# Optimization experiments

Measured on AMD Instinct MI355X. Metric: run time of the kernel, lower is better.

Reference implementation:

```python
import jax, jax.numpy as jnp
import numpy as np

B, L, E, H, NL = 2, 1024, 1024, 16, 3
D = E // H
SCALE = D ** -0.5
EPS = 1e-5


def rmsnorm(x, g):
    return x * jax.lax.rsqrt(jnp.mean(x * x, axis=-1, keepdims=True) + EPS) * g


def rope(x, cos, sin):
    # x: (B, m*L, H, D); cos/sin: (L, D). Tile cos/sin to the growing KV length
    # (the source broadcasts rel_pos over the concatenated cache).
    m = x.shape[1] // cos.shape[0]
    c = jnp.tile(cos, (m, 1))[None, :, None, :]
    s = jnp.tile(sin, (m, 1))[None, :, None, :]
    x1, x2 = jnp.split(x, 2, axis=-1)
    rot = jnp.concatenate([-x2, x1], axis=-1)  # rotate_half convention
    return x * c + rot * s


def setup_inputs() -> dict:
    key = jax.random.key(0)
    ks = jax.random.split(key, 8)
    x = jax.random.normal(ks[0], (B, L, E), jnp.float32)
    inv_freq = 1.0 / (10000.0 ** (jnp.arange(0, D, 2, dtype=jnp.float32) / D))
    t = jnp.arange(L, dtype=jnp.float32)[:, None] * inv_freq[None, :]  # (L, D/2)
    cos = jnp.concatenate([jnp.cos(t), jnp.cos(t)], axis=-1)
    sin = jnp.concatenate([jnp.sin(t), jnp.sin(t)], axis=-1)
    attn_mask = jnp.where(jnp.tril(jnp.ones((L, L), bool)), 0.0, -jnp.inf).astype(jnp.float32)
    w_scale = E ** -0.5  # ~kaiming_uniform fan_in magnitude
    Wq = jax.random.normal(ks[1], (NL, E, E), jnp.float32) * w_scale
    Wk = jax.random.normal(ks[2], (NL, E, E), jnp.float32) * w_scale
    Wv = jax.random.normal(ks[3], (NL, E, E), jnp.float32) * w_scale
    Wo = jax.random.normal(ks[4], (E, E), jnp.float32) * w_scale
    lambdas = jax.random.normal(ks[5], (NL,), jnp.float32)
    g_ln = jnp.ones((NL, E), jnp.float32)
    g_final = jnp.ones((E,), jnp.float32)
    alpha = jnp.ones((1,), jnp.float32)
    return dict(x=x, cos=cos, sin=sin, attn_mask=attn_mask, Wq=Wq, Wk=Wk, Wv=Wv,
                g_ln=g_ln, lambdas=lambdas, Wo=Wo, g_final=g_final, alpha=alpha)


def reference(x, cos, sin, attn_mask, Wq, Wk, Wv, g_ln, lambdas, Wo, g_final, alpha):
    # lambda weights: sigmoid then non-affine LayerNorm across the NL layers
    s = jax.nn.sigmoid(lambdas)
    lw = (s - s.mean()) * jax.lax.rsqrt(s.var() + EPS)

    acc_k, acc_v = [], []
    outs = []
    for i in range(NL):
        q = (x @ Wq[i].T).reshape(B, L, H, D)
        k = (x @ Wk[i].T).reshape(B, L, H, D)
        v = (x @ Wv[i].T).reshape(B, L, H, D)
        if i > 0:  # prepend-current growing KV cache (source concatenates [k, accumulated])
            k = jnp.concatenate([k] + acc_k, axis=1)
            v = jnp.concatenate([v] + acc_v, axis=1)
        q = rope(q, cos, sin)
        k = rope(k, cos, sin)
        KV = k.shape[1]
        scores = jnp.einsum('bqhd,bkhd->bhqk', q * SCALE, k)  # (B,H,L,KV)
        if i == 0:
            m = attn_mask
        else:  # source fills everything past tgt_len with -inf
            m = jnp.concatenate(
                [attn_mask, jnp.full((L, KV - L), -jnp.inf, attn_mask.dtype)], axis=1)
        w = jax.nn.softmax(scores + m, axis=-1)
        a = jnp.einsum('bhqk,bkhd->bqhd', w, v).reshape(B, L, E)
        outs.append(rmsnorm(a, g_ln[i]) * lw[i])
        acc_k.append(k)  # stores the full concatenated, roped k (lengths 1L,2L,4L)
        acc_v.append(v)
    combined = outs[0] + outs[1] + outs[2]
    out = rmsnorm(combined + alpha * x, g_final)
    return out @ Wo.T
```

## Files before the change

kernel.cpp:

```cpp
#include <hip/hip_runtime.h>


#define B_  2
#define L_  1024
#define E_  1024
#define H_  16
#define NL_ 3
#define D_  64

typedef __bf16 bf16_t;
typedef __bf16 bf16x8 __attribute__((ext_vector_type(8)));
typedef __bf16 bf16x4 __attribute__((ext_vector_type(4)));
typedef float  f32x4  __attribute__((ext_vector_type(4)));

#define NEG_INF (-__builtin_inff())

typedef const __attribute__((address_space(1))) void* gas_ptr;
typedef __attribute__((address_space(3))) void* las_ptr;

#define GLD_LDS16(gp, lp) \
  __builtin_amdgcn_global_load_lds((gas_ptr)(gp), (las_ptr)(lp), 16, 0, 0)

__global__ __launch_bounds__(256) void cvt_k(
    const float* __restrict__ s0, const float* __restrict__ s1,
    const float* __restrict__ s2, const float* __restrict__ s3,
    const float* __restrict__ s4, bf16_t* __restrict__ d0,
    bf16_t* __restrict__ d1, bf16_t* __restrict__ d2, bf16_t* __restrict__ d3,
    bf16_t* __restrict__ d4)
{
  const int seg = blockIdx.y;
  const float* s;
  bf16_t* d;
  int n;
  if (seg == 0)      { s = s0; d = d0; n = 3145728; }
  else if (seg == 1) { s = s1; d = d1; n = 3145728; }
  else if (seg == 2) { s = s2; d = d2; n = 3145728; }
  else if (seg == 3) { s = s3; d = d3; n = 1048576; }
  else               { s = s4; d = d4; n = 2097152; }
  const int i = (blockIdx.x * 256 + threadIdx.x) * 4;
  if (i < n) {
    const float4 v = *(const float4*)(s + i);
    bf16x4 o;
    o[0] = (bf16_t)v.x; o[1] = (bf16_t)v.y; o[2] = (bf16_t)v.z; o[3] = (bf16_t)v.w;
    *(bf16x4*)(d + i) = o;
  }
}

template <int EPI>
__global__ __launch_bounds__(256) void gemm_k(
    const bf16_t* __restrict__ X, const bf16_t* __restrict__ W0,
    const bf16_t* __restrict__ W1, const bf16_t* __restrict__ W2,
    const float* __restrict__ cosb, const float* __restrict__ sinb,
    bf16_t* __restrict__ qk, bf16_t* __restrict__ vt, float* __restrict__ outf)
{
  __shared__ bf16_t smem[128 * 128];
  bf16_t* Xs = smem;
  bf16_t* Ws = smem + 8192;
  const int tid = threadIdx.x;
  const int lane = tid & 63;
  const int w = tid >> 6;
  const int q4 = lane >> 4, l15 = lane & 15;
  const int l7 = l15 & 7;

  const int flat0 = blockIdx.y * 16 + blockIdx.x;
  const int chunk = (EPI ? 128 : 1152) >> 3;
  const int nf = (flat0 & 7) * chunk + (flat0 >> 3);
  const int bxs = nf & 15;
  const int bys = nf >> 4;

  const int row0 = bxs * 128;

  int g, tileN;
  const bf16_t* Wb;
  if (EPI == 0) {
    g = bys >> 3;
    tileN = bys & 7;
    const int t = g % 3, il = g / 3;
    Wb = (t == 0 ? W0 : (t == 1 ? W1 : W2)) + (size_t)il * E_ * E_;
  } else {
    g = 0;
    tileN = bys;
    Wb = W0;
  }
  const int col0 = tileN * 128;
  const int rA = (w & 1) * 64;
  const int cB = (w >> 1) * 64;

  const int srow = tid >> 3;
  const int scol = (((tid & 7) ^ (srow & 7)) << 3);

  f32x4 acc[4][4] = {};

  for (int k0 = 0; k0 < E_; k0 += 64) {
    __syncthreads();
#pragma unroll
    for (int it = 0; it < 4; ++it) {
      const int flat = it * 2048 + tid * 8;
      const int r = it * 32 + srow;
      GLD_LDS16(X + (size_t)(row0 + r) * E_ + k0 + scol, &Xs[flat]);
      GLD_LDS16(Wb + (size_t)(col0 + r) * E_ + k0 + scol, &Ws[flat]);
    }
    __syncthreads();
#pragma unroll
    for (int kk = 0; kk < 2; ++kk) {
      bf16x8 a[4], b[4];
      const int cg = ((kk * 4 + q4) ^ l7) << 3;
#pragma unroll
      for (int mi = 0; mi < 4; ++mi)
        a[mi] = *(const bf16x8*)&Xs[(rA + mi * 16 + l15) * 64 + cg];
#pragma unroll
      for (int ni = 0; ni < 4; ++ni)
        b[ni] = *(const bf16x8*)&Ws[(cB + ni * 16 + l15) * 64 + cg];
#pragma unroll
      for (int mi = 0; mi < 4; ++mi)
#pragma unroll
        for (int ni = 0; ni < 4; ++ni)
          acc[mi][ni] =
              __builtin_amdgcn_mfma_f32_16x16x32_bf16(a[mi], b[ni], acc[mi][ni], 0, 0, 0);
    }
  }

  if (EPI == 0) {
    const int t = g % 3, il = g / 3;
    if (t < 2) {
      const int slot = il * 2 + t;
      const int h = tileN * 2 + (w >> 1);
      const float post = (t == 0) ? 0.18033688011112042f : 1.0f;
#pragma unroll
      for (int mi = 0; mi < 4; ++mi) {
#pragma unroll
        for (int reg = 0; reg < 4; ++reg) {
          const int m = row0 + rA + mi * 16 + q4 * 4 + reg;
          const int b = m >> 10, l = m & (L_ - 1);
#pragma unroll
          for (int ni = 0; ni < 4; ++ni) {
            const int d = ni * 16 + l15;
            const float v0 = acc[mi][ni][reg];
            const float part = acc[mi][ni ^ 2][reg];
            const float rot = (d < 32) ? -part : part;
            const float v = (v0 * cosb[l * D_ + d] + rot * sinb[l * D_ + d]) * post;
            qk[(((size_t)slot * B_ + b) * H_ + h) * ((size_t)L_ * D_) +
               (size_t)l * D_ + d] = (bf16_t)v;
          }
        }
      }
    } else {
      const int n_l = tid >> 1, lh = tid & 1;
      const int h = tileN * 2 + (n_l >> 6), d = n_l & 63;
      const int bb = row0 >> 10;
      __syncthreads();
#pragma unroll
      for (int p = 0; p < 2; ++p) {
        if ((w & 1) == p) {
#pragma unroll
          for (int mi = 0; mi < 4; ++mi)
#pragma unroll
            for (int reg = 0; reg < 4; ++reg)
#pragma unroll
              for (int ni = 0; ni < 4; ++ni)
                smem[(cB + ni * 16 + l15) * 72 + mi * 16 + q4 * 4 + reg] =
                    (bf16_t)acc[mi][ni][reg];
        }
        __syncthreads();
        const int l0 = (row0 & (L_ - 1)) + p * 64 + lh * 32;
        bf16_t* gp = vt + (((size_t)il * B_ + bb) * H_ + h) * ((size_t)D_ * L_) +
                     (size_t)d * L_ + l0;
        const bf16_t* sp = &smem[n_l * 72 + lh * 32];
#pragma unroll
        for (int c = 0; c < 4; ++c)
          *(bf16x8*)(gp + c * 8) = *(const bf16x8*)(sp + c * 8);
        if (p == 0) __syncthreads();
      }
    }
  } else {
#pragma unroll
    for (int mi = 0; mi < 4; ++mi) {
#pragma unroll
      for (int reg = 0; reg < 4; ++reg) {
        const int m = row0 + rA + mi * 16 + q4 * 4 + reg;
#pragma unroll
        for (int ni = 0; ni < 4; ++ni) {
          const int n = col0 + cB + ni * 16 + l15;
          outf[(size_t)m * E_ + n] = acc[mi][ni][reg];
        }
      }
    }
  }
}

__global__ __launch_bounds__(256) void attn_k(const bf16_t* __restrict__ qk,
                                              const bf16_t* __restrict__ vt,
                                              bf16_t* __restrict__ attn)
{
  __shared__ bf16_t Ks[2][64 * 64];
  __shared__ bf16_t Vts[2][64 * 64];
  __shared__ bf16_t Ps[4][16 * 72];

  const int tid = threadIdx.x, lane = tid & 63, w = tid >> 6;
  const int q4 = lane >> 4, l15 = lane & 15;

  const int flat0 = blockIdx.y * 8 + blockIdx.x;
  const int nf = (flat0 & 7) * 96 + (flat0 >> 3);
  const int x = nf & 7;
  const int by = nf >> 3;

  const int h = by & 15, b = (by >> 4) & 1, i = by >> 5;
  const size_t HD = (size_t)L_ * D_;
  const bf16_t* Qp = qk + (((size_t)(i * 2 + 0) * B_ + b) * H_ + h) * HD;
  const bf16_t* Kp = qk + (((size_t)(i * 2 + 1) * B_ + b) * H_ + h) * HD;
  const bf16_t* Vp = vt + (((size_t)i * B_ + b) * H_ + h) * HD;

  const int srow = tid >> 3;
  const int sg = tid & 7;
  const int scol = (sg ^ (srow & 7)) * 8;

  bf16x8 ones;
#pragma unroll
  for (int jj = 0; jj < 8; ++jj) ones[jj] = (bf16_t)1.0f;

#pragma unroll 1
  for (int ph = 0; ph < 2; ++ph) {
    const int qt = ph == 0 ? (15 - x) : x;

    bf16x8 aq[2];
#pragma unroll
    for (int kk = 0; kk < 2; ++kk)
      aq[kk] = *(const bf16x8*)(Qp + (size_t)(qt * 64 + w * 16 + l15) * 64 +
                                kk * 32 + q4 * 8);

    if (ph == 1) __syncthreads();
#pragma unroll
    for (int it = 0; it < 2; ++it) {
      const int flat = it * 2048 + tid * 8;
      const int r = it * 32 + srow;
      GLD_LDS16(Kp + r * 64 + scol, &Ks[0][flat]);
      GLD_LDS16(Vp + (size_t)r * L_ + scol, &Vts[0][flat]);
    }

    f32x4 o[4] = {};
    f32x4 lacc = {};

#pragma unroll 1
    for (int j = 0; j <= qt; ++j) {
      __syncthreads();
      const int cur = j & 1;
      if (j < qt) {
        const int nxt = cur ^ 1;
#pragma unroll
        for (int it = 0; it < 2; ++it) {
          const int flat = it * 2048 + tid * 8;
          const int r = it * 32 + srow;
          GLD_LDS16(Kp + (j + 1) * 4096 + r * 64 + scol, &Ks[nxt][flat]);
          GLD_LDS16(Vp + (size_t)r * L_ + (j + 1) * 64 + scol, &Vts[nxt][flat]);
        }
      }

      f32x4 s[4] = {};
#pragma unroll
      for (int kk = 0; kk < 2; ++kk) {
#pragma unroll
        for (int ni = 0; ni < 4; ++ni) {
          const bf16x8 bk =
              *(const bf16x8*)&Ks[cur][(ni * 16 + l15) * 64 +
                                       (((kk * 4 + q4) ^ (l15 & 7)) << 3)];
          s[ni] = __builtin_amdgcn_mfma_f32_16x16x32_bf16(aq[kk], bk, s[ni], 0, 0, 0);
        }
      }

      if (j == qt) {
#pragma unroll
        for (int reg = 0; reg < 4; ++reg)
#pragma unroll
          for (int ni = 0; ni < 4; ++ni)
            if (ni * 16 + l15 > w * 16 + q4 * 4 + reg) s[ni][reg] = NEG_INF;
      }

#pragma unroll
      for (int reg = 0; reg < 4; ++reg)
#pragma unroll
        for (int ni = 0; ni < 4; ++ni)
          Ps[w][(q4 * 4 + reg) * 72 + ni * 16 + l15] = (bf16_t)exp2f(s[ni][reg]);
      asm volatile("s_waitcnt lgkmcnt(0)" ::: "memory");

#pragma unroll
      for (int kk = 0; kk < 2; ++kk) {
        const bf16x8 ap = *(const bf16x8*)&Ps[w][l15 * 72 + kk * 32 + q4 * 8];
        lacc = __builtin_amdgcn_mfma_f32_16x16x32_bf16(ap, ones, lacc, 0, 0, 0);
#pragma unroll
        for (int di = 0; di < 4; ++di) {
          const bf16x8 bv =
              *(const bf16x8*)&Vts[cur][(di * 16 + l15) * 64 +
                                        (((kk * 4 + q4) ^ (l15 & 7)) << 3)];
          o[di] = __builtin_amdgcn_mfma_f32_16x16x32_bf16(ap, bv, o[di], 0, 0, 0);
        }
      }
    }

    const int row_base = (i * B_ + b) * L_ + qt * 64 + w * 16 + q4 * 4;
#pragma unroll
    for (int reg = 0; reg < 4; ++reg) {
      const float inv = 1.f / lacc[reg];
      const int r = row_base + reg;
#pragma unroll
      for (int di = 0; di < 4; ++di)
        attn[(size_t)r * E_ + h * 64 + di * 16 + l15] = (bf16_t)(o[di][reg] * inv);
    }
  }
}

__device__ __forceinline__ float block_sum(float v, float* sm)
{
#pragma unroll
  for (int off = 32; off > 0; off >>= 1) v += __shfl_xor(v, off);
  const int w = threadIdx.x >> 6;
  __syncthreads();
  if ((threadIdx.x & 63) == 0) sm[w] = v;
  __syncthreads();
  return sm[0] + sm[1] + sm[2] + sm[3];
}

__global__ __launch_bounds__(256) void combine_k(
    const bf16_t* __restrict__ attn, const float* __restrict__ x,
    const float* __restrict__ g_ln, const float* __restrict__ lambdas,
    const float* __restrict__ g_final, const float* __restrict__ alphap,
    bf16_t* __restrict__ xn)
{
  __shared__ float sm[4];
  const int row = blockIdx.x;
  const int tid = threadIdx.x;

  float sg[3], lw[3];
#pragma unroll
  for (int i = 0; i < 3; ++i) sg[i] = 1.f / (1.f + expf(-lambdas[i]));
  const float mean = (sg[0] + sg[1] + sg[2]) * (1.f / 3.f);
  const float var = ((sg[0] - mean) * (sg[0] - mean) + (sg[1] - mean) * (sg[1] - mean) +
                     (sg[2] - mean) * (sg[2] - mean)) * (1.f / 3.f);
  const float rv = rsqrtf(var + 1e-5f);
#pragma unroll
  for (int i = 0; i < 3; ++i) lw[i] = (sg[i] - mean) * rv;

  const float av = alphap[0];
  float c[4];
#pragma unroll
  for (int k = 0; k < 4; ++k) {
    const int e = tid + k * 256;
    c[k] = av * x[(size_t)row * E_ + e];
  }

  for (int i = 0; i < 3; ++i) {
    float a[4];
    float ss = 0.f;
#pragma unroll
    for (int k = 0; k < 4; ++k) {
      const int e = tid + k * 256;
      a[k] = (float)attn[((size_t)i * (B_ * L_) + row) * E_ + e];
      ss += a[k] * a[k];
    }
    ss = block_sum(ss, sm);
    const float rinv = rsqrtf(ss * (1.f / (float)E_) + 1e-5f);
#pragma unroll
    for (int k = 0; k < 4; ++k) {
      const int e = tid + k * 256;
      c[k] += a[k] * rinv * g_ln[i * E_ + e] * lw[i];
    }
  }

  float ss = 0.f;
#pragma unroll
  for (int k = 0; k < 4; ++k) ss += c[k] * c[k];
  ss = block_sum(ss, sm);
  const float rinv = rsqrtf(ss * (1.f / (float)E_) + 1e-5f);
#pragma unroll
  for (int k = 0; k < 4; ++k) {
    const int e = tid + k * 256;
    xn[(size_t)row * E_ + e] = (bf16_t)(c[k] * rinv * g_final[e]);
  }
}

extern "C" void kernel_launch(void* const* d_in, const int* in_sizes, int n_in,
                              void* d_out, int out_size, void* d_ws, size_t ws_size,
                              hipStream_t stream)
{
  const float* x       = (const float*)d_in[0];
  const float* cosb    = (const float*)d_in[1];
  const float* sinb    = (const float*)d_in[2];
  const float* Wq      = (const float*)d_in[4];
  const float* Wk      = (const float*)d_in[5];
  const float* Wv      = (const float*)d_in[6];
  const float* g_ln    = (const float*)d_in[7];
  const float* lambdas = (const float*)d_in[8];
  const float* Wo      = (const float*)d_in[9];
  const float* g_final = (const float*)d_in[10];
  const float* alphap  = (const float*)d_in[11];

  bf16_t* qk    = (bf16_t*)d_ws;
  bf16_t* VT    = (bf16_t*)((char*)d_ws + 25165824);
  bf16_t* attnb = (bf16_t*)((char*)d_ws + 37748736);
  bf16_t* Wqb   = (bf16_t*)((char*)d_ws + 50331648);
  bf16_t* Wkb   = Wqb + 3145728;
  bf16_t* Wvb   = Wkb + 3145728;
  bf16_t* Wob   = (bf16_t*)((char*)d_ws + 69206016);
  bf16_t* xb    = (bf16_t*)((char*)d_ws + 71303168);
  bf16_t* xnb   = (bf16_t*)d_ws;
  float*  out   = (float*)d_out;

  cvt_k<<<dim3(3072, 5), 256, 0, stream>>>(Wq, Wk, Wv, Wo, x, Wqb, Wkb, Wvb, Wob, xb);
  gemm_k<0><<<dim3(16, 72), 256, 0, stream>>>(xb, Wqb, Wkb, Wvb, cosb, sinb,
                                              qk, VT, nullptr);
  attn_k<<<dim3(8, 96), 256, 0, stream>>>(qk, VT, attnb);
  combine_k<<<dim3(B_ * L_), 256, 0, stream>>>(attnb, x, g_ln, lambdas, g_final,
                                               alphap, xnb);
  gemm_k<1><<<dim3(16, 8), 256, 0, stream>>>(xnb, Wob, Wob, Wob, cosb, sinb,
                                             nullptr, nullptr, out);
}
```

Baseline: 237.0 us.

## Double-buffer GEMM LDS tiles with K=32 steps to overlap loads and MFMA

The GEMM main loop now uses two LDS buffers of 128x32 tiles for X and W. The next tile is issued via global_load_lds while MFMAs run on the current one, so there is one barrier per step instead of two. The swizzle is rewritten for the 32-wide rows. The cost is a smaller K step, which means twice as many iterations and barriers, and possible LDS bank conflicts under the new swizzle.

```diff
diff --git a/kernel.cpp b/kernel.cpp
--- a/kernel.cpp
+++ b/kernel.cpp
@@ -54,13 +54,11 @@
     bf16_t* __restrict__ qk, bf16_t* __restrict__ vt, float* __restrict__ outf)
 {
   __shared__ bf16_t smem[128 * 128];
-  bf16_t* Xs = smem;
-  bf16_t* Ws = smem + 8192;
   const int tid = threadIdx.x;
   const int lane = tid & 63;
   const int w = tid >> 6;
   const int q4 = lane >> 4, l15 = lane & 15;
-  const int l7 = l15 & 7;
+  const int row0swz = (l15 >> 1) & 3;
 
   const int flat0 = blockIdx.y * 16 + blockIdx.x;
   const int chunk = (EPI ? 128 : 1152) >> 3;
@@ -86,39 +84,59 @@
   const int rA = (w & 1) * 64;
   const int cB = (w >> 1) * 64;
 
-  const int srow = tid >> 3;
-  const int scol = (((tid & 7) ^ (srow & 7)) << 3);
+  const int srow = tid >> 2;
+  const int sgcol = (((tid & 3) ^ ((tid >> 3) & 3)) << 3);
 
   f32x4 acc[4][4] = {};
 
-  for (int k0 = 0; k0 < E_; k0 += 64) {
+  const size_t xrow = (size_t)(row0 + srow) * E_ + sgcol;
+  const size_t xrow2 = xrow + (size_t)64 * E_;
+  const size_t wrow = (size_t)(col0 + srow) * E_ + sgcol;
+  const size_t wrow2 = wrow + (size_t)64 * E_;
+
+#define STAGE_(buf, k0_)                                         \
+  do {                                                           \
+    bf16_t* Xb = smem + (buf) * 8192;                            \
+    bf16_t* Wbl = smem + (buf) * 8192 + 4096;                    \
+    GLD_LDS16(X + xrow + (k0_), &Xb[tid * 8]);                   \
+    GLD_LDS16(X + xrow2 + (k0_), &Xb[2048 + tid * 8]);           \
+    GLD_LDS16(Wb + wrow + (k0_), &Wbl[tid * 8]);                 \
+    GLD_LDS16(Wb + wrow2 + (k0_), &Wbl[2048 + tid * 8]);         \
+  } while (0)
+
+#define COMPUTE_(buf)                                            \
+  do {                                                           \
+    const bf16_t* Xb = smem + (buf) * 8192;                      \
+    const bf16_t* Wbl = smem + (buf) * 8192 + 4096;              \
+    bf16x8 a[4], b[4];                                           \
+    const int slot = (q4 ^ row0swz) << 3;                        \
+    _Pragma("unroll")                                            \
+    for (int mi = 0; mi < 4; ++mi)                               \
+      a[mi] = *(const bf16x8*)&Xb[(rA + mi * 16 + l15) * 32 + slot]; \
+    _Pragma("unroll")                                            \
+    for (int ni = 0; ni < 4; ++ni)                               \
+      b[ni] = *(const bf16x8*)&Wbl[(cB + ni * 16 + l15) * 32 + slot]; \
+    _Pragma("unroll")                                            \
+    for (int mi = 0; mi < 4; ++mi)                               \
+      _Pragma("unroll")                                          \
+      for (int ni = 0; ni < 4; ++ni)                             \
+        acc[mi][ni] = __builtin_amdgcn_mfma_f32_16x16x32_bf16(   \
+            a[mi], b[ni], acc[mi][ni], 0, 0, 0);                 \
+  } while (0)
+
+  STAGE_(0, 0);
+  __syncthreads();
+  int cur = 0;
+  for (int k0 = 32; k0 < E_; k0 += 32) {
+    STAGE_(cur ^ 1, k0);
+    COMPUTE_(cur);
     __syncthreads();
-#pragma unroll
-    for (int it = 0; it < 4; ++it) {
-      const int flat = it * 2048 + tid * 8;
-      const int r = it * 32 + srow;
-      GLD_LDS16(X + (size_t)(row0 + r) * E_ + k0 + scol, &Xs[flat]);
-      GLD_LDS16(Wb + (size_t)(col0 + r) * E_ + k0 + scol, &Ws[flat]);
-    }
-    __syncthreads();
-#pragma unroll
-    for (int kk = 0; kk < 2; ++kk) {
-      bf16x8 a[4], b[4];
-      const int cg = ((kk * 4 + q4) ^ l7) << 3;
-#pragma unroll
-      for (int mi = 0; mi < 4; ++mi)
-        a[mi] = *(const bf16x8*)&Xs[(rA + mi * 16 + l15) * 64 + cg];
-#pragma unroll
-      for (int ni = 0; ni < 4; ++ni)
-        b[ni] = *(const bf16x8*)&Ws[(cB + ni * 16 + l15) * 64 + cg];
-#pragma unroll
-      for (int mi = 0; mi < 4; ++mi)
-#pragma unroll
-        for (int ni = 0; ni < 4; ++ni)
-          acc[mi][ni] =
-              __builtin_amdgcn_mfma_f32_16x16x32_bf16(a[mi], b[ni], acc[mi][ni], 0, 0, 0);
-    }
-  }
+    cur ^= 1;
+  }
+  COMPUTE_(cur);
+
+#undef STAGE_
+#undef COMPUTE_
 
   if (EPI == 0) {
     const int t = g % 3, il = g / 3;
```

Result: no change. 235.3 us (-0.7%).
